# Kernel optimization log

Measured on AMD Instinct MI355X. Metric: run time of the kernel, lower is better.

Reference implementation:

```python
import jax, jax.numpy as jnp
import numpy as np

H = 16          # num heads
DH = 64         # head size
D = H * DH      # hidden size 1024
B, S = 2, 2048


def setup_inputs() -> dict:
    key = jax.random.key(0)
    ks = jax.random.split(key, 9)
    scale = 1.0 / np.sqrt(D)
    p = {}
    p["hidden_states"] = jax.random.normal(ks[0], (B, S, D), dtype=jnp.float32)
    for i, name in enumerate(["q", "k", "v", "o"]):
        # stored so that y = x @ W + b (transpose of torch Linear weight)
        p[f"W{name}"] = jax.random.normal(ks[1 + 2 * i], (D, D), dtype=jnp.float32) * scale
        p[f"b{name}"] = jax.random.normal(ks[2 + 2 * i], (D,), dtype=jnp.float32) * 0.01
    return p


def reference(hidden_states, Wq, bq, Wk, bk, Wv, bv, Wo, bo):
    b, s, _ = hidden_states.shape
    q = hidden_states @ Wq + bq  # [B,S,D]
    k = hidden_states @ Wk + bk
    v = hidden_states @ Wv + bv
    # [B,H,S,DH]
    q = q.reshape(b, s, H, DH).transpose(0, 2, 1, 3)
    k = k.reshape(b, s, H, DH).transpose(0, 2, 1, 3)
    v = v.reshape(b, s, H, DH).transpose(0, 2, 1, 3)
    scores = jnp.einsum("bhqd,bhkd->bhqk", q, k) / np.sqrt(DH)
    causal = jnp.triu(jnp.ones((s, s), dtype=bool), k=1)  # True above diagonal -> masked
    scores = jnp.where(causal, -jnp.inf, scores)
    attn = jax.nn.softmax(scores, axis=-1)  # dropout p=0 (eval)
    ctx = jnp.einsum("bhqk,bhkd->bhqd", attn, v)
    ctx = ctx.transpose(0, 2, 1, 3).reshape(b, s, D)
    return ctx @ Wo + bo
```

## Files before the change

kernel.cpp:

```cpp
#include <hip/hip_runtime.h>


typedef _Float16 f16x8 __attribute__((ext_vector_type(8)));
typedef _Float16 f16x4 __attribute__((ext_vector_type(4)));
typedef float f32x4 __attribute__((ext_vector_type(4)));

#define GLD_LDS16(g, l)                                                        \
  __builtin_amdgcn_global_load_lds(                                            \
      (__attribute__((address_space(1))) const unsigned int*)(g),              \
      (__attribute__((address_space(3))) unsigned int*)(l), 16, 0, 0)

static constexpr int Sdim = 2048;
static constexpr int Ddim = 1024;
static constexpr int NH = 16;
static constexpr int DH = 64;
static constexpr int Mrows = 4096;

static constexpr float QSCALE = 0.125f * 1.44269504f;
static constexpr float SHIFT = 4.0f;

__global__ __launch_bounds__(256) void xcvt(const float* __restrict__ X,
                                            _Float16* __restrict__ Y) {
  size_t i = ((size_t)blockIdx.x * 256 + threadIdx.x) * 8;
  float4 f0 = *(const float4*)(X + i);
  float4 f1 = *(const float4*)(X + i + 4);
  alignas(16) _Float16 h[8] = {(_Float16)f0.x, (_Float16)f0.y, (_Float16)f0.z,
                               (_Float16)f0.w, (_Float16)f1.x, (_Float16)f1.y,
                               (_Float16)f1.z, (_Float16)f1.w};
  *(uint4*)(Y + i) = *(const uint4*)h;
}

struct WtArgs {
  const float *s0, *s1, *s2, *s3;
  _Float16 *d0, *d1, *d2, *d3;
};

__global__ __launch_bounds__(256) void wtrans(WtArgs a) {
  __shared__ _Float16 L[64 * 72];
  const int z = blockIdx.z;
  const float* src = z == 0 ? a.s0 : z == 1 ? a.s1 : z == 2 ? a.s2 : a.s3;
  _Float16* dst = z == 0 ? a.d0 : z == 1 ? a.d1 : z == 2 ? a.d2 : a.d3;
  const int k0 = blockIdx.x * 64, n0 = blockIdx.y * 64, t = threadIdx.x;
#pragma unroll
  for (int i = 0; i < 4; ++i) {
    int c = i * 256 + t;
    int row = c >> 4, cc = c & 15;
    float4 f = *(const float4*)&src[(size_t)(k0 + row) * Ddim + n0 + cc * 4];
    L[(cc * 4 + 0) * 72 + row] = (_Float16)f.x;
    L[(cc * 4 + 1) * 72 + row] = (_Float16)f.y;
    L[(cc * 4 + 2) * 72 + row] = (_Float16)f.z;
    L[(cc * 4 + 3) * 72 + row] = (_Float16)f.w;
  }
  __syncthreads();
#pragma unroll
  for (int i = 0; i < 2; ++i) {
    int c = i * 256 + t;
    int n = c >> 3, cc = c & 7;
    *(uint4*)&dst[(size_t)(n0 + n) * Ddim + k0 + cc * 8] =
        *(const uint4*)&L[n * 72 + cc * 8];
  }
}

struct GemmArgs {
  const _Float16* A;
  const _Float16 *Bt0, *Bt1, *Bt2;
  const float *b0, *b1, *b2;
  void *o0, *o1, *o2;
};

template <int MODE>
__global__ __launch_bounds__(256) void gemm128(GemmArgs g) {
  constexpr int K = 1024;
  __shared__ _Float16 As[128 * 32];
  __shared__ _Float16 Bs[128 * 32];
  const int z = blockIdx.z;
  const _Float16* A = g.A;
  const _Float16* Bt = z == 0 ? g.Bt0 : z == 1 ? g.Bt1 : g.Bt2;
  const float* bias = z == 0 ? g.b0 : z == 1 ? g.b1 : g.b2;
  void* out = z == 0 ? g.o0 : z == 1 ? g.o1 : g.o2;
  const int m0 = blockIdx.x * 128, n0 = blockIdx.y * 128;
  const int t = threadIdx.x, lane = t & 63, wv = t >> 6;
  const int wm = wv >> 1, wn = wv & 1, quad = lane >> 4, r = lane & 15;

  const int c0 = wv * 64 + lane, c1 = c0 + 256;
  const _Float16* ga0 = A + (size_t)(m0 + (c0 >> 2)) * K + (c0 & 3) * 8;
  const _Float16* ga1 = A + (size_t)(m0 + (c1 >> 2)) * K + (c1 & 3) * 8;
  const _Float16* gb0 = Bt + (size_t)(n0 + (c0 >> 2)) * K + (c0 & 3) * 8;
  const _Float16* gb1 = Bt + (size_t)(n0 + (c1 >> 2)) * K + (c1 & 3) * 8;
  char* lA0 = (char*)As + (wv * 64) * 16;
  char* lA1 = (char*)As + (256 + wv * 64) * 16;
  char* lB0 = (char*)Bs + (wv * 64) * 16;
  char* lB1 = (char*)Bs + (256 + wv * 64) * 16;

  f32x4 acc[4][4] = {};
  for (int kt = 0; kt < K; kt += 32) {
    GLD_LDS16(ga0 + kt, lA0);
    GLD_LDS16(ga1 + kt, lA1);
    GLD_LDS16(gb0 + kt, lB0);
    GLD_LDS16(gb1 + kt, lB1);
    __syncthreads();
    f16x8 af[4], bf[4];
#pragma unroll
    for (int mi = 0; mi < 4; ++mi)
      af[mi] = *(const f16x8*)&As[(wm * 64 + mi * 16 + r) * 32 + quad * 8];
#pragma unroll
    for (int ni = 0; ni < 4; ++ni)
      bf[ni] = *(const f16x8*)&Bs[(wn * 64 + ni * 16 + r) * 32 + quad * 8];
#pragma unroll
    for (int mi = 0; mi < 4; ++mi)
#pragma unroll
      for (int ni = 0; ni < 4; ++ni)
        acc[mi][ni] = __builtin_amdgcn_mfma_f32_16x16x32_f16(af[mi], bf[ni],
                                                             acc[mi][ni], 0, 0, 0);
    __syncthreads();
  }

  const float scale = (MODE == 0 && z == 0) ? QSCALE : 1.0f;
  float bv[4];
#pragma unroll
  for (int ni = 0; ni < 4; ++ni) bv[ni] = bias[n0 + wn * 64 + ni * 16 + r];
#pragma unroll
  for (int mi = 0; mi < 4; ++mi) {
#pragma unroll
    for (int ni = 0; ni < 4; ++ni) {
      const int n = n0 + wn * 64 + ni * 16 + r;
      if (MODE == 0 && z == 2) {
        alignas(8) _Float16 h4[4];
#pragma unroll
        for (int reg = 0; reg < 4; ++reg)
          h4[reg] = (_Float16)(acc[mi][ni][reg] + bv[ni]);
        const int m = m0 + wm * 64 + mi * 16 + quad * 4;
        const int b = m >> 11, s = m & 2047, h = n >> 6, dh = n & 63;
        *(uint2*)&((_Float16*)out)[((size_t)(b * NH + h) * DH + dh) * Sdim + s] =
            *(const uint2*)h4;
      } else {
#pragma unroll
        for (int reg = 0; reg < 4; ++reg) {
          const int m = m0 + wm * 64 + mi * 16 + quad * 4 + reg;
          const float v = (acc[mi][ni][reg] + bv[ni]) * scale;
          if (MODE == 0) {
            const int b = m >> 11, s = m & 2047, h = n >> 6, dh = n & 63;
            ((_Float16*)out)[(((size_t)(b * NH + h) * Sdim + s) << 6) + dh] =
                (_Float16)v;
          } else {
            ((float*)out)[(size_t)m * Ddim + n] = v;
          }
        }
      }
    }
  }
}

__global__ __launch_bounds__(256) void attn(const _Float16* __restrict__ Q,
                                            const _Float16* __restrict__ Kk,
                                            const _Float16* __restrict__ Vt,
                                            _Float16* __restrict__ ctx) {
  constexpr int LDK = 72;
  __shared__ _Float16 Ks[2][64 * LDK], Vs[2][64 * LDK], Ps[4 * 16 * LDK];
  const int id = blockIdx.x, xcd = id & 7, slot = id >> 3;
  const int x = slot & 15, bh = ((slot >> 4) << 3) | xcd;
  const int t = threadIdx.x, lane = t & 63, wv = t >> 6;
  const int quad = lane >> 4, r = lane & 15;
  const _Float16* Kg = Kk + (size_t)bh * Sdim * DH;
  const _Float16* Vg = Vt + (size_t)bh * DH * Sdim;
  _Float16* Pw = Ps + wv * 16 * LDK;
  const int b = bh >> 4, h = bh & 15;
  const int sr0 = t >> 3, sc0 = (t & 7) * 8, sr1 = (t + 256) >> 3;

#pragma unroll
  for (int pass = 0; pass < 2; ++pass) {
    const int qt = pass == 0 ? x : 31 - x;
    const int q0 = qt * 64;
    const _Float16* Qrow = Q + ((size_t)bh * Sdim + q0 + wv * 16 + r) * DH;
    const f16x8 aq0 = *(const f16x8*)(Qrow + quad * 8);
    const f16x8 aq1 = *(const f16x8*)(Qrow + 32 + quad * 8);
    const int qcol = q0 + wv * 16 + r;

    float l_i = 0.f;
    f32x4 oacc[4] = {};

    const int ntiles = qt + 1;
    uint4 ka = *(const uint4*)&Kg[(size_t)sr0 * DH + sc0];
    uint4 kb = *(const uint4*)&Kg[(size_t)sr1 * DH + sc0];
    uint4 va = *(const uint4*)&Vg[(size_t)sr0 * Sdim + sc0];
    uint4 vb = *(const uint4*)&Vg[(size_t)sr1 * Sdim + sc0];
    __syncthreads();
    *(uint4*)&Ks[0][sr0 * LDK + sc0] = ka;
    *(uint4*)&Ks[0][sr1 * LDK + sc0] = kb;
    *(uint4*)&Vs[0][sr0 * LDK + sc0] = va;
    *(uint4*)&Vs[0][sr1 * LDK + sc0] = vb;

    for (int it = 0; it < ntiles; ++it) {
      const int cur = it & 1;
      if (it + 1 < ntiles) {
        const int kvn = (it + 1) * 64;
        ka = *(const uint4*)&Kg[(size_t)(kvn + sr0) * DH + sc0];
        kb = *(const uint4*)&Kg[(size_t)(kvn + sr1) * DH + sc0];
        va = *(const uint4*)&Vg[(size_t)sr0 * Sdim + kvn + sc0];
        vb = *(const uint4*)&Vg[(size_t)sr1 * Sdim + kvn + sc0];
      }
      __syncthreads();

      f32x4 sacc[4] = {};
#pragma unroll
      for (int ks = 0; ks < 2; ++ks) {
        const f16x8 bq = ks ? aq1 : aq0;
#pragma unroll
        for (int ni = 0; ni < 4; ++ni) {
          f16x8 ak =
              *(const f16x8*)&Ks[cur][(ni * 16 + r) * LDK + ks * 32 + quad * 8];
          sacc[ni] =
              __builtin_amdgcn_mfma_f32_16x16x32_f16(ak, bq, sacc[ni], 0, 0, 0);
        }
      }

      const bool diag = (it == ntiles - 1);
      const int kvb = it * 64;
      float lp = 0.f;
#pragma unroll
      for (int ni = 0; ni < 4; ++ni) {
        alignas(8) f16x4 h4;
#pragma unroll
        for (int reg = 0; reg < 4; ++reg) {
          float sv = sacc[ni][reg];
          if (diag && (kvb + ni * 16 + quad * 4 + reg > qcol)) sv = -1e30f;
          const float p = exp2f(sv - SHIFT);
          lp += p;
          h4[reg] = (_Float16)p;
        }
        *(f16x4*)&Pw[r * LDK + ni * 16 + quad * 4] = h4;
      }
      lp += __shfl_xor(lp, 16, 64);
      lp += __shfl_xor(lp, 32, 64);
      l_i += lp;

#pragma unroll
      for (int ks = 0; ks < 2; ++ks) {
        f16x8 ap = *(const f16x8*)&Pw[r * LDK + ks * 32 + quad * 8];
#pragma unroll
        for (int ni = 0; ni < 4; ++ni) {
          f16x8 bv =
              *(const f16x8*)&Vs[cur][(ni * 16 + r) * LDK + ks * 32 + quad * 8];
          oacc[ni] =
              __builtin_amdgcn_mfma_f32_16x16x32_f16(ap, bv, oacc[ni], 0, 0, 0);
        }
      }

      if (it + 1 < ntiles) {
        const int nxt = cur ^ 1;
        *(uint4*)&Ks[nxt][sr0 * LDK + sc0] = ka;
        *(uint4*)&Ks[nxt][sr1 * LDK + sc0] = kb;
        *(uint4*)&Vs[nxt][sr0 * LDK + sc0] = va;
        *(uint4*)&Vs[nxt][sr1 * LDK + sc0] = vb;
      }
    }

#pragma unroll
    for (int reg = 0; reg < 4; ++reg) {
      const float lq = __shfl(l_i, quad * 4 + reg, 16);
      const float rl = 1.0f / lq;
      const int qrow = q0 + wv * 16 + quad * 4 + reg;
#pragma unroll
      for (int ni = 0; ni < 4; ++ni) {
        ctx[((size_t)b * Sdim + qrow) * Ddim + h * DH + ni * 16 + r] =
            (_Float16)(oacc[ni][reg] * rl);
      }
    }
  }
}

extern "C" void kernel_launch(void* const* d_in, const int* in_sizes, int n_in,
                              void* d_out, int out_size, void* d_ws,
                              size_t ws_size, hipStream_t stream) {
  const float* hid = (const float*)d_in[0];
  const float* Wq = (const float*)d_in[1];
  const float* bq = (const float*)d_in[2];
  const float* Wk = (const float*)d_in[3];
  const float* bk = (const float*)d_in[4];
  const float* Wv = (const float*)d_in[5];
  const float* bv = (const float*)d_in[6];
  const float* Wo = (const float*)d_in[7];
  const float* bo = (const float*)d_in[8];

  char* ws = (char*)d_ws;
  _Float16* Xh = (_Float16*)(ws);
  _Float16* Wqt = (_Float16*)(ws + (8ull << 20));
  _Float16* Wkt = (_Float16*)(ws + (10ull << 20));
  _Float16* Wvt = (_Float16*)(ws + (12ull << 20));
  _Float16* Wot = (_Float16*)(ws + (14ull << 20));
  _Float16* Qb = (_Float16*)(ws + (16ull << 20));
  _Float16* Kb = (_Float16*)(ws + (24ull << 20));
  _Float16* Vtb = (_Float16*)(ws + (32ull << 20));
  _Float16* ctx = Xh;

  xcvt<<<dim3(Mrows * Ddim / (256 * 8)), 256, 0, stream>>>(hid, Xh);

  WtArgs wa{Wq, Wk, Wv, Wo, Wqt, Wkt, Wvt, Wot};
  wtrans<<<dim3(16, 16, 4), 256, 0, stream>>>(wa);

  GemmArgs g1{Xh, Wqt, Wkt, Wvt, bq, bk, bv, Qb, Kb, Vtb};
  gemm128<0><<<dim3(Mrows / 128, Ddim / 128, 3), 256, 0, stream>>>(g1);

  attn<<<dim3(512), 256, 0, stream>>>(Qb, Kb, Vtb, ctx);

  GemmArgs g2{ctx, Wot, Wot, Wot, bo, bo, bo, d_out, d_out, d_out};
  gemm128<1><<<dim3(Mrows / 128, Ddim / 128, 1), 256, 0, stream>>>(g2);
}
```

Baseline: 191.4 us.

## Rewrite attention with 32x32 MFMA, 128-row query tiles and XOR-swizzled LDS

The attention kernel moves from 16x16x32 MFMAs over 64-query tiles to 32x32x16 MFMAs over 128-query tiles, with interleaved query rows spread across the four waves. The two-pass causal load balancing is dropped and each block handles one tile, scheduled largest-first. Padded LDS rows are replaced by XOR-swizzled 64-wide rows, s_setprio is placed around the MFMA sections, and the fixed softmax shift is removed. The aim is fewer MFMA and LDS instructions per FLOP and better reuse of K/V tiles, at the cost of more registers per wave and possibly worse causal load balance. Without the shift, exp2 of unshifted scores could overflow fp16 for large scores.

```diff
diff --git a/kernel.cpp b/kernel.cpp
--- a/kernel.cpp
+++ b/kernel.cpp
@@ -4,6 +4,7 @@
 typedef _Float16 f16x8 __attribute__((ext_vector_type(8)));
 typedef _Float16 f16x4 __attribute__((ext_vector_type(4)));
 typedef float f32x4 __attribute__((ext_vector_type(4)));
+typedef float f32x16 __attribute__((ext_vector_type(16)));
 
 #define GLD_LDS16(g, l)                                                        \
   __builtin_amdgcn_global_load_lds(                                            \
@@ -17,7 +18,6 @@
 static constexpr int Mrows = 4096;
 
 static constexpr float QSCALE = 0.125f * 1.44269504f;
-static constexpr float SHIFT = 4.0f;
 
 __global__ __launch_bounds__(256) void xcvt(const float* __restrict__ X,
                                             _Float16* __restrict__ Y) {
@@ -155,117 +155,126 @@
                                             const _Float16* __restrict__ Kk,
                                             const _Float16* __restrict__ Vt,
                                             _Float16* __restrict__ ctx) {
-  constexpr int LDK = 72;
-  __shared__ _Float16 Ks[2][64 * LDK], Vs[2][64 * LDK], Ps[4 * 16 * LDK];
+  __shared__ _Float16 Ks[2][64 * 64], Vs[2][64 * 64], Ps[4][32 * 64];
   const int id = blockIdx.x, xcd = id & 7, slot = id >> 3;
-  const int x = slot & 15, bh = ((slot >> 4) << 3) | xcd;
+  const int grp = slot >> 4, ti = slot & 15;
+  const int bh = (grp << 3) | xcd;
+  const int qt = 15 - ti;
   const int t = threadIdx.x, lane = t & 63, wv = t >> 6;
-  const int quad = lane >> 4, r = lane & 15;
+  const int q = lane & 31, qb = q & 7, h5 = lane >> 5, h8 = h5 * 8;
+  const int b = bh >> 4, h = bh & 15;
   const _Float16* Kg = Kk + (size_t)bh * Sdim * DH;
   const _Float16* Vg = Vt + (size_t)bh * DH * Sdim;
-  _Float16* Pw = Ps + wv * 16 * LDK;
-  const int b = bh >> 4, h = bh & 15;
-  const int sr0 = t >> 3, sc0 = (t & 7) * 8, sr1 = (t + 256) >> 3;
-
-#pragma unroll
-  for (int pass = 0; pass < 2; ++pass) {
-    const int qt = pass == 0 ? x : 31 - x;
-    const int q0 = qt * 64;
-    const _Float16* Qrow = Q + ((size_t)bh * Sdim + q0 + wv * 16 + r) * DH;
-    const f16x8 aq0 = *(const f16x8*)(Qrow + quad * 8);
-    const f16x8 aq1 = *(const f16x8*)(Qrow + 32 + quad * 8);
-    const int qcol = q0 + wv * 16 + r;
-
-    float l_i = 0.f;
-    f32x4 oacc[4] = {};
-
-    const int ntiles = qt + 1;
-    uint4 ka = *(const uint4*)&Kg[(size_t)sr0 * DH + sc0];
-    uint4 kb = *(const uint4*)&Kg[(size_t)sr1 * DH + sc0];
-    uint4 va = *(const uint4*)&Vg[(size_t)sr0 * Sdim + sc0];
-    uint4 vb = *(const uint4*)&Vg[(size_t)sr1 * Sdim + sc0];
+  _Float16* Pw = Ps[wv];
+
+  const int qa = qt * 128 + (q >> 3) * 32 + wv * 8 + qb;
+  const int qmin = qt * 128 + wv * 8;
+
+  const _Float16* Qrow = Q + ((size_t)bh * Sdim + qa) * DH;
+  f16x8 aq[4];
+#pragma unroll
+  for (int ks = 0; ks < 4; ++ks) aq[ks] = *(const f16x8*)(Qrow + ks * 16 + h8);
+
+  const int ntiles = 2 * qt + 2;
+  const int sr0 = t >> 3, sr1 = sr0 + 32, sc = (t & 7) * 8;
+  const int wc0 = sc ^ ((sr0 & 7) << 3), wc1 = sc ^ ((sr1 & 7) << 3);
+
+  f32x16 oacc0 = {}, oacc1 = {};
+  float l_i = 0.f;
+
+  uint4 ka = *(const uint4*)&Kg[(size_t)sr0 * DH + sc];
+  uint4 kb = *(const uint4*)&Kg[(size_t)sr1 * DH + sc];
+  uint4 va = *(const uint4*)&Vg[(size_t)sr0 * Sdim + sc];
+  uint4 vb = *(const uint4*)&Vg[(size_t)sr1 * Sdim + sc];
+  *(uint4*)&Ks[0][sr0 * 64 + wc0] = ka;
+  *(uint4*)&Ks[0][sr1 * 64 + wc1] = kb;
+  *(uint4*)&Vs[0][sr0 * 64 + wc0] = va;
+  *(uint4*)&Vs[0][sr1 * 64 + wc1] = vb;
+
+  for (int it = 0; it < ntiles; ++it) {
+    const int cur = it & 1;
+    if (it + 1 < ntiles) {
+      const int kvn = (it + 1) * 64;
+      ka = *(const uint4*)&Kg[(size_t)(kvn + sr0) * DH + sc];
+      kb = *(const uint4*)&Kg[(size_t)(kvn + sr1) * DH + sc];
+      va = *(const uint4*)&Vg[(size_t)sr0 * Sdim + kvn + sc];
+      vb = *(const uint4*)&Vg[(size_t)sr1 * Sdim + kvn + sc];
+    }
     __syncthreads();
-    *(uint4*)&Ks[0][sr0 * LDK + sc0] = ka;
-    *(uint4*)&Ks[0][sr1 * LDK + sc0] = kb;
-    *(uint4*)&Vs[0][sr0 * LDK + sc0] = va;
-    *(uint4*)&Vs[0][sr1 * LDK + sc0] = vb;
-
-    for (int it = 0; it < ntiles; ++it) {
-      const int cur = it & 1;
-      if (it + 1 < ntiles) {
-        const int kvn = (it + 1) * 64;
-        ka = *(const uint4*)&Kg[(size_t)(kvn + sr0) * DH + sc0];
-        kb = *(const uint4*)&Kg[(size_t)(kvn + sr1) * DH + sc0];
-        va = *(const uint4*)&Vg[(size_t)sr0 * Sdim + kvn + sc0];
-        vb = *(const uint4*)&Vg[(size_t)sr1 * Sdim + kvn + sc0];
+
+    f32x16 s0 = {}, s1 = {};
+    __builtin_amdgcn_s_setprio(1);
+#pragma unroll
+    for (int ks = 0; ks < 4; ++ks) {
+      const int co = (ks * 16 + h8) ^ (qb << 3);
+      f16x8 ak0 = *(const f16x8*)&Ks[cur][q * 64 + co];
+      f16x8 ak1 = *(const f16x8*)&Ks[cur][(32 + q) * 64 + co];
+      s0 = __builtin_amdgcn_mfma_f32_32x32x16_f16(ak0, aq[ks], s0, 0, 0, 0);
+      s1 = __builtin_amdgcn_mfma_f32_32x32x16_f16(ak1, aq[ks], s1, 0, 0, 0);
+    }
+    __builtin_amdgcn_s_setprio(0);
+
+    const int kvb = it * 64;
+    const bool msk = (kvb + 63 > qmin);
+    float lp = 0.f;
+#pragma unroll
+    for (int mb = 0; mb < 2; ++mb) {
+      const f32x16 sv = mb ? s1 : s0;
+      const int kv0 = kvb + mb * 32 + 4 * h5;
+#pragma unroll
+      for (int g = 0; g < 4; ++g) {
+        alignas(8) f16x4 h4;
+#pragma unroll
+        for (int c = 0; c < 4; ++c) {
+          float x = sv[g * 4 + c];
+          if (msk && (kv0 + 8 * g + c > qa)) x = -1e30f;
+          const float p = exp2f(x);
+          lp += p;
+          h4[c] = (_Float16)p;
+        }
+        *(f16x4*)&Pw[q * 64 + ((mb * 32 + 8 * g + 4 * h5) ^ (qb << 3))] = h4;
       }
-      __syncthreads();
-
-      f32x4 sacc[4] = {};
-#pragma unroll
-      for (int ks = 0; ks < 2; ++ks) {
-        const f16x8 bq = ks ? aq1 : aq0;
-#pragma unroll
-        for (int ni = 0; ni < 4; ++ni) {
-          f16x8 ak =
-              *(const f16x8*)&Ks[cur][(ni * 16 + r) * LDK + ks * 32 + quad * 8];
-          sacc[ni] =
-              __builtin_amdgcn_mfma_f32_16x16x32_f16(ak, bq, sacc[ni], 0, 0, 0);
-        }
-      }
-
-      const bool diag = (it == ntiles - 1);
-      const int kvb = it * 64;
-      float lp = 0.f;
-#pragma unroll
-      for (int ni = 0; ni < 4; ++ni) {
-        alignas(8) f16x4 h4;
-#pragma unroll
-        for (int reg = 0; reg < 4; ++reg) {
-          float sv = sacc[ni][reg];
-          if (diag && (kvb + ni * 16 + quad * 4 + reg > qcol)) sv = -1e30f;
-          const float p = exp2f(sv - SHIFT);
-          lp += p;
-          h4[reg] = (_Float16)p;
-        }
-        *(f16x4*)&Pw[r * LDK + ni * 16 + quad * 4] = h4;
-      }
-      lp += __shfl_xor(lp, 16, 64);
-      lp += __shfl_xor(lp, 32, 64);
-      l_i += lp;
-
-#pragma unroll
-      for (int ks = 0; ks < 2; ++ks) {
-        f16x8 ap = *(const f16x8*)&Pw[r * LDK + ks * 32 + quad * 8];
-#pragma unroll
-        for (int ni = 0; ni < 4; ++ni) {
-          f16x8 bv =
-              *(const f16x8*)&Vs[cur][(ni * 16 + r) * LDK + ks * 32 + quad * 8];
-          oacc[ni] =
-              __builtin_amdgcn_mfma_f32_16x16x32_f16(ap, bv, oacc[ni], 0, 0, 0);
-        }
-      }
-
-      if (it + 1 < ntiles) {
-        const int nxt = cur ^ 1;
-        *(uint4*)&Ks[nxt][sr0 * LDK + sc0] = ka;
-        *(uint4*)&Ks[nxt][sr1 * LDK + sc0] = kb;
-        *(uint4*)&Vs[nxt][sr0 * LDK + sc0] = va;
-        *(uint4*)&Vs[nxt][sr1 * LDK + sc0] = vb;
-      }
-    }
-
-#pragma unroll
-    for (int reg = 0; reg < 4; ++reg) {
-      const float lq = __shfl(l_i, quad * 4 + reg, 16);
-      const float rl = 1.0f / lq;
-      const int qrow = q0 + wv * 16 + quad * 4 + reg;
-#pragma unroll
-      for (int ni = 0; ni < 4; ++ni) {
-        ctx[((size_t)b * Sdim + qrow) * Ddim + h * DH + ni * 16 + r] =
-            (_Float16)(oacc[ni][reg] * rl);
-      }
-    }
+    }
+    lp += __shfl_xor(lp, 32, 64);
+    l_i += lp;
+
+    f16x8 ap[4];
+#pragma unroll
+    for (int ks = 0; ks < 4; ++ks)
+      ap[ks] = *(const f16x8*)&Pw[q * 64 + ((ks * 16 + h8) ^ (qb << 3))];
+    __builtin_amdgcn_s_setprio(1);
+#pragma unroll
+    for (int ks = 0; ks < 4; ++ks) {
+      const int co = (ks * 16 + h8) ^ (qb << 3);
+      f16x8 bv0 = *(const f16x8*)&Vs[cur][q * 64 + co];
+      f16x8 bv1 = *(const f16x8*)&Vs[cur][(32 + q) * 64 + co];
+      oacc0 = __builtin_amdgcn_mfma_f32_32x32x16_f16(ap[ks], bv0, oacc0, 0, 0, 0);
+      oacc1 = __builtin_amdgcn_mfma_f32_32x32x16_f16(ap[ks], bv1, oacc1, 0, 0, 0);
+    }
+    __builtin_amdgcn_s_setprio(0);
+
+    if (it + 1 < ntiles) {
+      const int nxt = cur ^ 1;
+      *(uint4*)&Ks[nxt][sr0 * 64 + wc0] = ka;
+      *(uint4*)&Ks[nxt][sr1 * 64 + wc1] = kb;
+      *(uint4*)&Vs[nxt][sr0 * 64 + wc0] = va;
+      *(uint4*)&Vs[nxt][sr1 * 64 + wc1] = vb;
+    }
+  }
+
+  float rl[16];
+#pragma unroll
+  for (int rr = 0; rr < 16; ++rr) {
+    const int qi = (rr & 3) + 8 * (rr >> 2) + 4 * h5;
+    rl[rr] = 1.0f / __shfl(l_i, qi, 64);
+  }
+#pragma unroll
+  for (int rr = 0; rr < 16; ++rr) {
+    const int qi = (rr & 3) + 8 * (rr >> 2) + 4 * h5;
+    const int s = qt * 128 + (qi >> 3) * 32 + wv * 8 + (qi & 7);
+    const size_t base = ((size_t)b * Sdim + s) * Ddim + h * DH;
+    ctx[base + q] = (_Float16)(oacc0[rr] * rl[rr]);
+    ctx[base + 32 + q] = (_Float16)(oacc1[rr] * rl[rr]);
   }
 }
 
```

Measured after the change: 220.8 us. +15.4%, slower.
